# Kernel optimization log

Measured on AMD Instinct MI355X. Metric: run time of the kernel, lower is better.

The kernel has to match this reference:

```python
import jax, jax.numpy as jnp
import numpy as np

N_HEAD = 16
ROPE_BASE = 10000.0
RMS_EPS = 1e-6

def rms_norm(x):
    # F.rms_norm(x, (x.size(-1),)) -- no learned weight
    return x * jax.lax.rsqrt(jnp.mean(x * x, axis=-1, keepdims=True) + RMS_EPS)

def rope(x):
    # x: [B, T, H, hd]; rotate halves (non-interleaved) like the torch Rotary
    T, hd = x.shape[1], x.shape[3]
    d = hd // 2
    inv_freq = 1.0 / (ROPE_BASE ** (jnp.arange(0, hd, 2, dtype=jnp.float32) / hd))  # [d]
    t = jnp.arange(T, dtype=jnp.float32)
    freqs = jnp.outer(t, inv_freq)                       # [T, d]
    cos = jnp.cos(freqs)[None, :, None, :]
    sin = jnp.sin(freqs)[None, :, None, :]
    x1, x2 = x[..., :d], x[..., d:]
    y1 = x1 * cos + x2 * sin
    y2 = -x1 * sin + x2 * cos
    return jnp.concatenate([y1, y2], axis=-1).astype(x.dtype)

def setup_inputs() -> dict:
    key = jax.random.key(0)
    ks = jax.random.split(key, 7)
    B, T, D, H = 2, 2048, 1024, N_HEAD
    hd = D // H
    s = 0.02
    return {
        "x": jax.random.normal(ks[0], (B, T, D), jnp.float32),
        "v1": jax.random.normal(ks[1], (B, T, H, hd), jnp.float32),
        "w_q": jax.random.normal(ks[2], (D, D), jnp.float32) * s,
        "w_k": jax.random.normal(ks[3], (D, D), jnp.float32) * s,
        "w_v": jax.random.normal(ks[4], (D, D), jnp.float32) * s,
        "w_proj": jax.random.normal(ks[5], (D, D), jnp.float32) * s,
        "lamb": jnp.float32(0.5),
    }

def reference(x, v1, w_q, w_k, w_v, w_proj, lamb):
    B, T, D = x.shape
    H = N_HEAD
    hd = D // H
    q = (x @ w_q.T).reshape(B, T, H, hd)
    k = (x @ w_k.T).reshape(B, T, H, hd)
    v = (x @ w_v.T).reshape(B, T, H, hd)
    v = (1.0 - lamb) * v + lamb * v1.reshape(B, T, H, hd)
    q, k = rms_norm(q), rms_norm(k)
    q, k = rope(q), rope(k)
    scale = 1.0 / jnp.sqrt(jnp.float32(hd))
    scores = jnp.einsum('bqhd,bkhd->bhqk', q, k) * scale  # [B,H,T,T]
    causal = jnp.tril(jnp.ones((T, T), dtype=bool))
    scores = jnp.where(causal[None, None], scores, jnp.float32(-1e30))
    attn = jax.nn.softmax(scores, axis=-1)
    y = jnp.einsum('bhqk,bkhd->bqhd', attn, v).reshape(B, T, D)
    y = y @ w_proj.T
    return (y, v1)
```

## Files before the change

### kernel.cpp

```cpp
#include <hip/hip_runtime.h>

typedef __bf16 bf16x8 __attribute__((ext_vector_type(8)));
typedef float f32x4 __attribute__((ext_vector_type(4)));
typedef float f32x16 __attribute__((ext_vector_type(16)));

__device__ __forceinline__ unsigned short f2bf(float f) {
    return __builtin_bit_cast(unsigned short, (__bf16)f);
}

__device__ __forceinline__ float bf2f(unsigned short u) {
    unsigned int x = ((unsigned int)u) << 16;
    return __builtin_bit_cast(float, x);
}

__device__ __forceinline__ unsigned int packbf2(float a, float b) {
    unsigned short lo = f2bf(a), hi = f2bf(b);
    return (unsigned int)lo | ((unsigned int)hi << 16);
}

__device__ __forceinline__ bf16x8 load_frag(const unsigned short* p) {
    int4 v = *reinterpret_cast<const int4*>(p);
    return __builtin_bit_cast(bf16x8, v);
}

__device__ __forceinline__ void gload_lds16(const unsigned short* g, unsigned short* l) {
    __builtin_amdgcn_global_load_lds((const __attribute__((address_space(1))) void*)g,
                                     (__attribute__((address_space(3))) void*)l, 16, 0, 0);
}

__global__ __launch_bounds__(256) void prep_bf16(const float* __restrict__ x,
                                                 const float* __restrict__ wq,
                                                 const float* __restrict__ wk,
                                                 const float* __restrict__ wv,
                                                 const float* __restrict__ wp,
                                                 unsigned short* __restrict__ xb,
                                                 unsigned short* __restrict__ wall,
                                                 float* __restrict__ cost,
                                                 float* __restrict__ sint) {
    int bid = blockIdx.x;
    if (bid < 8192) {
        int i = (bid * 256 + threadIdx.x) * 4;
        const float* src;
        unsigned short* dst;
        int soff, doff;
        if (i < (1 << 22)) {
            src = x; dst = xb; soff = i; doff = i;
        } else {
            int j = i - (1 << 22);
            int r = j >> 20;
            src = (r == 0) ? wq : ((r == 1) ? wk : ((r == 2) ? wv : wp));
            dst = wall; soff = j & 1048575; doff = j;
        }
        float4 v = *reinterpret_cast<const float4*>(&src[soff]);
        unsigned short tmp[4] = {f2bf(v.x), f2bf(v.y), f2bf(v.z), f2bf(v.w)};
        *reinterpret_cast<int2*>(&dst[doff]) = *reinterpret_cast<int2*>(tmp);
    } else {
        int i = (bid - 8192) * 256 + threadIdx.x;
        int t = i >> 5, d = i & 31;
        float inv = powf(10000.0f, -(float)d / 32.0f);
        float f = (float)t * inv;
        cost[i] = cosf(f);
        sint[i] = sinf(f);
    }
}

__global__ __launch_bounds__(256) void gemm_qkv(const unsigned short* __restrict__ A,
                                                const unsigned short* __restrict__ B,
                                                const float* __restrict__ cost,
                                                const float* __restrict__ sint,
                                                const float* __restrict__ v1,
                                                const float* __restrict__ lamb_p,
                                                unsigned short* __restrict__ qb,
                                                unsigned short* __restrict__ kb,
                                                unsigned short* __restrict__ vbv,
                                                float* __restrict__ outv1) {
    __shared__ __align__(16) unsigned short As[128 * 64];
    __shared__ __align__(16) unsigned short Bs[128 * 64];
    int tid = threadIdx.x;
    int lane = tid & 63;
    int w = tid >> 6;
    int wm = w >> 1, wn = w & 1;
    int m0 = blockIdx.x * 128;
    int n0 = blockIdx.y * 128;

    f32x4 acc[4][4] = {};

    int r8 = lane >> 3;
    int csrc = (lane & 7) ^ r8;

    for (int k0 = 0; k0 < 1024; k0 += 64) {
        __syncthreads();
#pragma unroll
        for (int c = 0; c < 4; ++c) {
            int row = 32 * w + 8 * c + r8;
            gload_lds16(&A[(size_t)(m0 + row) * 1024 + k0 + csrc * 8], &As[(32 * w + 8 * c) * 64]);
            gload_lds16(&B[(size_t)(n0 + row) * 1024 + k0 + csrc * 8], &Bs[(32 * w + 8 * c) * 64]);
        }
        __syncthreads();
#pragma unroll
        for (int kk = 0; kk < 2; ++kk) {
            int col16 = kk * 4 + (lane >> 4);
            bf16x8 af[4], bfr[4];
#pragma unroll
            for (int i = 0; i < 4; ++i) {
                int row = wm * 64 + i * 16 + (lane & 15);
                af[i] = load_frag(&As[row * 64 + (col16 ^ (row & 7)) * 8]);
            }
#pragma unroll
            for (int j = 0; j < 4; ++j) {
                int row = wn * 64 + j * 16 + (lane & 15);
                bfr[j] = load_frag(&Bs[row * 64 + (col16 ^ (row & 7)) * 8]);
            }
#pragma unroll
            for (int i = 0; i < 4; ++i)
#pragma unroll
                for (int j = 0; j < 4; ++j)
                    acc[i][j] = __builtin_amdgcn_mfma_f32_16x16x32_bf16(af[i], bfr[j], acc[i][j], 0, 0, 0);
        }
    }

    int r0 = (lane >> 4) * 4;
    int cc = lane & 15;
    int sec = blockIdx.y >> 3;
    int hh = (blockIdx.y & 7) * 2 + wn;

    if (sec < 2) {
        unsigned short* dst = (sec == 0) ? qb : kb;
        float sc = (sec == 0) ? (0.125f * 1.44269504088896f) : 1.0f;
#pragma unroll
        for (int i = 0; i < 4; ++i)
#pragma unroll
            for (int r = 0; r < 4; ++r) {
                float ss = 0.0f;
#pragma unroll
                for (int j = 0; j < 4; ++j) ss += acc[i][j][r] * acc[i][j][r];
                ss += __shfl_xor(ss, 1, 64);
                ss += __shfl_xor(ss, 2, 64);
                ss += __shfl_xor(ss, 4, 64);
                ss += __shfl_xor(ss, 8, 64);
                float rn = rsqrtf(ss * (1.0f / 64.0f) + 1e-6f);
                int mm = m0 + wm * 64 + i * 16 + r0 + r;
                int t = mm & 2047, b = mm >> 11;
                size_t rowb = ((size_t)((b * 16 + hh) * 2048 + t)) * 64;
#pragma unroll
                for (int j = 0; j < 2; ++j) {
                    int dm = j * 16 + cc;
                    float c = cost[t * 32 + dm], s_ = sint[t * 32 + dm];
                    float x1 = acc[i][j][r] * rn;
                    float x2 = acc[i][j + 2][r] * rn;
                    dst[rowb + dm]      = f2bf((x1 * c + x2 * s_) * sc);
                    dst[rowb + 32 + dm] = f2bf((x2 * c - x1 * s_) * sc);
                }
            }
    } else {
        float lam = lamb_p[0];
        float oml = 1.0f - lam;
#pragma unroll
        for (int i = 0; i < 4; ++i)
#pragma unroll
            for (int r = 0; r < 4; ++r) {
                int mm = m0 + wm * 64 + i * 16 + r0 + r;
                int t = mm & 2047, b = mm >> 11;
                size_t v1row = ((size_t)((b * 2048 + t) * 16 + hh)) * 64;
                size_t vbrow = ((size_t)((b * 16 + hh) * 2048 + t)) * 64;
#pragma unroll
                for (int j = 0; j < 4; ++j) {
                    int d = j * 16 + cc;
                    float v1v = v1[v1row + d];
                    outv1[v1row + d] = v1v;
                    vbv[vbrow + d] = f2bf(oml * acc[i][j][r] + lam * v1v);
                }
            }
    }
}

__global__ __launch_bounds__(256) void transpose_v(const unsigned short* __restrict__ vbv,
                                                   unsigned short* __restrict__ vt) {
    __shared__ __align__(16) unsigned short tile[64][72];
    int bid = blockIdx.x;
    int bh = bid >> 5;
    int t0 = (bid & 31) * 64;
    int tid = threadIdx.x;
    int r = tid >> 3;
    int c = (tid & 7) * 8;
    const unsigned short* src = vbv + ((size_t)bh * 2048 + t0) * 64;
    *reinterpret_cast<int4*>(&tile[r][c]) =
        *reinterpret_cast<const int4*>(&src[(size_t)r * 64 + c]);
    *reinterpret_cast<int4*>(&tile[r + 32][c]) =
        *reinterpret_cast<const int4*>(&src[(size_t)(r + 32) * 64 + c]);
    __syncthreads();
    unsigned short* dst = vt + (size_t)bh * 64 * 2048 + t0;
    unsigned short tmp[8];
#pragma unroll
    for (int j = 0; j < 8; ++j) tmp[j] = tile[c + j][r];
    *reinterpret_cast<int4*>(&dst[(size_t)r * 2048 + c]) = *reinterpret_cast<int4*>(tmp);
#pragma unroll
    for (int j = 0; j < 8; ++j) tmp[j] = tile[c + j][r + 32];
    *reinterpret_cast<int4*>(&dst[(size_t)(r + 32) * 2048 + c]) = *reinterpret_cast<int4*>(tmp);
}

__global__ __launch_bounds__(256) void gemm_proj(const unsigned short* __restrict__ pO,
                                                 const float* __restrict__ lsum,
                                                 const unsigned short* __restrict__ B,
                                                 float* __restrict__ C) {
    __shared__ __align__(16) unsigned short As[128 * 64];
    __shared__ __align__(16) unsigned short Bs[128 * 64];
    int tid = threadIdx.x;
    int lane = tid & 63;
    int w = tid >> 6;
    int wm = w >> 1, wn = w & 1;
    int m0 = blockIdx.x * 128;
    int n0 = blockIdx.y * 128;

    f32x4 acc[4][4] = {};

    int r8 = lane >> 3;
    int c8 = lane & 7;
    int csrc = c8 ^ r8;

    for (int k0 = 0; k0 < 1024; k0 += 64) {
        int h = k0 >> 6;
        __syncthreads();
#pragma unroll
        for (int c = 0; c < 4; ++c) {
            int row = 32 * w + 8 * c + r8;
            int m = m0 + row;
            int bh = ((m >> 11) << 4) + h;
            int qi = m & 2047;
            int li = bh * 2048 + qi;
            size_t pi = (size_t)li * 64 + csrc * 8;
            int4 p0 = *reinterpret_cast<const int4*>(&pO[pi]);
            int4 p1 = *reinterpret_cast<const int4*>(&pO[4194304u + pi]);
            float linv = 1.0f / (lsum[li] + lsum[65536 + li]);
            const unsigned short* u0 = reinterpret_cast<const unsigned short*>(&p0);
            const unsigned short* u1 = reinterpret_cast<const unsigned short*>(&p1);
            unsigned short tmp[8];
#pragma unroll
            for (int j = 0; j < 8; ++j) tmp[j] = f2bf((bf2f(u0[j]) + bf2f(u1[j])) * linv);
            *reinterpret_cast<int4*>(&As[row * 64 + c8 * 8]) = *reinterpret_cast<int4*>(tmp);
            gload_lds16(&B[(size_t)(n0 + row) * 1024 + k0 + csrc * 8], &Bs[(32 * w + 8 * c) * 64]);
        }
        __syncthreads();
#pragma unroll
        for (int kk = 0; kk < 2; ++kk) {
            int col16 = kk * 4 + (lane >> 4);
            bf16x8 af[4], bfr[4];
#pragma unroll
            for (int i = 0; i < 4; ++i) {
                int row = wm * 64 + i * 16 + (lane & 15);
                af[i] = load_frag(&As[row * 64 + (col16 ^ (row & 7)) * 8]);
            }
#pragma unroll
            for (int j = 0; j < 4; ++j) {
                int row = wn * 64 + j * 16 + (lane & 15);
                bfr[j] = load_frag(&Bs[row * 64 + (col16 ^ (row & 7)) * 8]);
            }
#pragma unroll
            for (int i = 0; i < 4; ++i)
#pragma unroll
                for (int j = 0; j < 4; ++j)
                    acc[i][j] = __builtin_amdgcn_mfma_f32_16x16x32_bf16(af[i], bfr[j], acc[i][j], 0, 0, 0);
        }
    }
    int r0 = (lane >> 4) * 4;
    int cc = lane & 15;
#pragma unroll
    for (int i = 0; i < 4; ++i)
#pragma unroll
        for (int j = 0; j < 4; ++j)
#pragma unroll
            for (int r = 0; r < 4; ++r) {
                size_t m = m0 + wm * 64 + i * 16 + r0 + r;
                size_t n = n0 + wn * 64 + j * 16 + cc;
                C[m * 1024 + n] = acc[i][j][r];
            }
}

__global__ __launch_bounds__(256) void attn(const unsigned short* __restrict__ qb,
                                            const unsigned short* __restrict__ kb,
                                            const unsigned short* __restrict__ vt,
                                            unsigned short* __restrict__ pO,
                                            float* __restrict__ lsum) {
    __shared__ __align__(16) unsigned short Ks[64][72];
    __shared__ __align__(16) unsigned short Vt[64][72];
    int tid = threadIdx.x;
    int lane = tid & 63;
    int w = tid >> 6;
    int hi = lane >> 5;
    int l31 = lane & 31;

    int bid = blockIdx.x;
    int bh = bid & 31;
    int r5 = bid >> 5;
    int qt = 15 - (r5 >> 1);
    int ck = r5 & 1;
    int q0 = qt * 128;
    const size_t base = (size_t)bh * 2048 * 64;
    const unsigned short* vtb = vt + (size_t)bh * 64 * 2048;
    int ktlo = ck * (qt + 1);
    int kthi = (ck + 1) * (qt + 1);

    bf16x8 qf[4];
    int qrow = q0 + w * 32 + l31;
#pragma unroll
    for (int kd = 0; kd < 4; ++kd)
        qf[kd] = load_frag(&qb[base + (size_t)qrow * 64 + kd * 16 + hi * 8]);

    f32x16 oacc[2] = {};
    float lrun = 0.0f;

    int srow = tid >> 3;
    int scol = (tid & 7) * 8;
    int4 kr0, kr1, vr0, vr1;
#define LOADT(kt_)                                                                                    \
    do {                                                                                              \
        kr0 = *reinterpret_cast<const int4*>(&kb[base + (size_t)((kt_)*64 + srow) * 64 + scol]);      \
        kr1 = *reinterpret_cast<const int4*>(&kb[base + (size_t)((kt_)*64 + srow + 32) * 64 + scol]); \
        vr0 = *reinterpret_cast<const int4*>(&vtb[(size_t)srow * 2048 + (kt_)*64 + scol]);            \
        vr1 = *reinterpret_cast<const int4*>(&vtb[(size_t)(srow + 32) * 2048 + (kt_)*64 + scol]);     \
    } while (0)

    int qwlo = q0 + w * 32;
    {
        LOADT(ktlo);
        for (int kt = ktlo; kt < kthi; ++kt) {
            __syncthreads();
            *reinterpret_cast<int4*>(&Ks[srow][scol]) = kr0;
            *reinterpret_cast<int4*>(&Ks[srow + 32][scol]) = kr1;
            *reinterpret_cast<int4*>(&Vt[srow][scol]) = vr0;
            *reinterpret_cast<int4*>(&Vt[srow + 32][scol]) = vr1;
            __syncthreads();
            if (kt + 1 < kthi) LOADT(kt + 1);

            if (kt * 64 <= qwlo + 31) {
                bool diag = (kt * 64 + 63 > qwlo);
                float rs01 = 0.0f, rs23 = 0.0f;
#pragma unroll
                for (int ntl = 0; ntl < 2; ++ntl) {
                    f32x16 sacc = {};
#pragma unroll
                    for (int kd = 0; kd < 4; ++kd) {
                        bf16x8 kf = load_frag(&Ks[ntl * 32 + l31][kd * 16 + hi * 8]);
                        sacc = __builtin_amdgcn_mfma_f32_32x32x16_bf16(kf, qf[kd], sacc, 0, 0, 0);
                    }

#pragma unroll
                    for (int r = 0; r < 16; ++r) {
                        float s = sacc[r];
                        if (diag) {
                            int kvg = kt * 64 + ntl * 32 + (r & 3) + 8 * (r >> 2) + 4 * hi;
                            if (kvg > qrow) s = -3.0e38f;
                        }
                        float e = __builtin_amdgcn_exp2f(s);
                        sacc[r] = e;
                        if (r & 2) rs23 += e; else rs01 += e;
                    }

                    unsigned int wAa[4], wBb[4];
#pragma unroll
                    for (int rr = 0; rr < 4; ++rr) {
                        wAa[rr] = packbf2(sacc[4 * rr + 0], sacc[4 * rr + 1]);
                        wBb[rr] = packbf2(sacc[4 * rr + 2], sacc[4 * rr + 3]);
                    }

#pragma unroll
                    for (int ks2 = 0; ks2 < 2; ++ks2) {
                        int b2 = ks2 * 2;
                        auto rA = __builtin_amdgcn_permlane32_swap(wAa[b2], wAa[b2 + 1], false, false);
                        auto rB = __builtin_amdgcn_permlane32_swap(wBb[b2], wBb[b2 + 1], false, false);
                        uint4 pa;
                        pa.x = rA[0];
                        pa.y = rB[0];
                        pa.z = rA[1];
                        pa.w = rB[1];
                        bf16x8 paf = __builtin_bit_cast(bf16x8, pa);
                        int ks = ntl * 2 + ks2;
#pragma unroll
                        for (int dt = 0; dt < 2; ++dt) {
                            bf16x8 vtf = load_frag(&Vt[dt * 32 + l31][ks * 16 + hi * 8]);
                            oacc[dt] = __builtin_amdgcn_mfma_f32_32x32x16_bf16(paf, vtf, oacc[dt], 0, 0, 0);
                        }
                    }
                }
                float rs = rs01 + rs23;
                rs += __shfl_xor(rs, 32, 64);
                lrun += rs;
            }
        }
    }

    unsigned short* po = pO + ((size_t)ck * 4194304u);
    float* ls = lsum + ck * 65536;
#pragma unroll
    for (int r = 0; r < 16; ++r) {
        int ql = (r & 3) + 8 * (r >> 2) + 4 * hi;
        int q = q0 + w * 32 + ql;
        size_t ro = ((size_t)bh * 2048 + q) * 64;
        po[ro + l31]      = f2bf(oacc[0][r]);
        po[ro + 32 + l31] = f2bf(oacc[1][r]);
    }
    if (hi == 0) ls[bh * 2048 + q0 + w * 32 + l31] = lrun;
#undef LOADT
}

extern "C" void kernel_launch(void* const* d_in, const int* in_sizes, int n_in,
                              void* d_out, int out_size, void* d_ws, size_t ws_size,
                              hipStream_t stream) {
    const float* x      = (const float*)d_in[0];
    const float* v1     = (const float*)d_in[1];
    const float* w_q    = (const float*)d_in[2];
    const float* w_k    = (const float*)d_in[3];
    const float* w_v    = (const float*)d_in[4];
    const float* w_proj = (const float*)d_in[5];
    const float* lamb   = (const float*)d_in[6];
    float* out = (float*)d_out;

    char* ws = (char*)d_ws;
    unsigned short* xb      = (unsigned short*)(ws + 0);
    unsigned short* wall_b  = (unsigned short*)(ws + (8u  << 20));
    unsigned short* wqkv_b  = wall_b;
    unsigned short* wproj_b = wall_b + 3u * 1048576u;
    unsigned short* vbuf    = (unsigned short*)(ws + (16u << 20));
    unsigned short* vtp     = (unsigned short*)(ws + (40u << 20));
    unsigned short* qbuf    = (unsigned short*)(ws + (48u << 20));
    unsigned short* kbuf    = (unsigned short*)(ws + (56u << 20));
    float*          cost    = (float*)        (ws + (72u << 20));
    float*          sint    = (float*)        (ws + (72u << 20) + 262144);
    unsigned short* pO      = (unsigned short*)(ws + (80u << 20));
    float*          lsum    = (float*)        (ws + (112u << 20));

    prep_bf16<<<8448, 256, 0, stream>>>(x, w_q, w_k, w_v, w_proj, xb, wall_b, cost, sint);

    gemm_qkv<<<dim3(32, 24), 256, 0, stream>>>(xb, wqkv_b, cost, sint, v1, lamb,
                                               qbuf, kbuf, vbuf, out + 4194304);

    transpose_v<<<1024, 256, 0, stream>>>(vbuf, vtp);

    attn<<<1024, 256, 0, stream>>>(qbuf, kbuf, vtp, pO, lsum);

    gemm_proj<<<dim3(32, 8), 256, 0, stream>>>(pO, lsum, wproj_b, out);
}
```

Baseline: 130.5 us.

## Fuse V transpose into a dedicated V projection GEMM epilogue

Splits the combined QKV GEMM into a Q/K GEMM and a separate V GEMM whose epilogue mixes in v1, stages the result in shared memory, and writes V directly in transposed layout. This removes the standalone transpose kernel and the intermediate V buffer round trip through global memory. In exchange the V GEMM runs as its own launch with only 256 blocks, which may underfill the GPU, and the epilogue adds an LDS staging pass and extra barriers.

```diff
diff --git a/kernel.cpp b/kernel.cpp
--- a/kernel.cpp
+++ b/kernel.cpp
@@ -64,16 +64,12 @@
     }
 }
 
-__global__ __launch_bounds__(256) void gemm_qkv(const unsigned short* __restrict__ A,
-                                                const unsigned short* __restrict__ B,
-                                                const float* __restrict__ cost,
-                                                const float* __restrict__ sint,
-                                                const float* __restrict__ v1,
-                                                const float* __restrict__ lamb_p,
-                                                unsigned short* __restrict__ qb,
-                                                unsigned short* __restrict__ kb,
-                                                unsigned short* __restrict__ vbv,
-                                                float* __restrict__ outv1) {
+__global__ __launch_bounds__(256) void gemm_qk(const unsigned short* __restrict__ A,
+                                               const unsigned short* __restrict__ B,
+                                               const float* __restrict__ cost,
+                                               const float* __restrict__ sint,
+                                               unsigned short* __restrict__ qb,
+                                               unsigned short* __restrict__ kb) {
     __shared__ __align__(16) unsigned short As[128 * 64];
     __shared__ __align__(16) unsigned short Bs[128 * 64];
     int tid = threadIdx.x;
@@ -123,80 +119,131 @@
     int cc = lane & 15;
     int sec = blockIdx.y >> 3;
     int hh = (blockIdx.y & 7) * 2 + wn;
-
-    if (sec < 2) {
-        unsigned short* dst = (sec == 0) ? qb : kb;
-        float sc = (sec == 0) ? (0.125f * 1.44269504088896f) : 1.0f;
-#pragma unroll
-        for (int i = 0; i < 4; ++i)
-#pragma unroll
-            for (int r = 0; r < 4; ++r) {
-                float ss = 0.0f;
-#pragma unroll
-                for (int j = 0; j < 4; ++j) ss += acc[i][j][r] * acc[i][j][r];
-                ss += __shfl_xor(ss, 1, 64);
-                ss += __shfl_xor(ss, 2, 64);
-                ss += __shfl_xor(ss, 4, 64);
-                ss += __shfl_xor(ss, 8, 64);
-                float rn = rsqrtf(ss * (1.0f / 64.0f) + 1e-6f);
-                int mm = m0 + wm * 64 + i * 16 + r0 + r;
-                int t = mm & 2047, b = mm >> 11;
-                size_t rowb = ((size_t)((b * 16 + hh) * 2048 + t)) * 64;
-#pragma unroll
-                for (int j = 0; j < 2; ++j) {
-                    int dm = j * 16 + cc;
-                    float c = cost[t * 32 + dm], s_ = sint[t * 32 + dm];
-                    float x1 = acc[i][j][r] * rn;
-                    float x2 = acc[i][j + 2][r] * rn;
-                    dst[rowb + dm]      = f2bf((x1 * c + x2 * s_) * sc);
-                    dst[rowb + 32 + dm] = f2bf((x2 * c - x1 * s_) * sc);
-                }
-            }
-    } else {
-        float lam = lamb_p[0];
-        float oml = 1.0f - lam;
-#pragma unroll
-        for (int i = 0; i < 4; ++i)
-#pragma unroll
-            for (int r = 0; r < 4; ++r) {
-                int mm = m0 + wm * 64 + i * 16 + r0 + r;
-                int t = mm & 2047, b = mm >> 11;
-                size_t v1row = ((size_t)((b * 2048 + t) * 16 + hh)) * 64;
-                size_t vbrow = ((size_t)((b * 16 + hh) * 2048 + t)) * 64;
-#pragma unroll
-                for (int j = 0; j < 4; ++j) {
-                    int d = j * 16 + cc;
-                    float v1v = v1[v1row + d];
-                    outv1[v1row + d] = v1v;
-                    vbv[vbrow + d] = f2bf(oml * acc[i][j][r] + lam * v1v);
-                }
-            }
-    }
-}
-
-__global__ __launch_bounds__(256) void transpose_v(const unsigned short* __restrict__ vbv,
-                                                   unsigned short* __restrict__ vt) {
-    __shared__ __align__(16) unsigned short tile[64][72];
-    int bid = blockIdx.x;
-    int bh = bid >> 5;
-    int t0 = (bid & 31) * 64;
+    unsigned short* dst = (sec == 0) ? qb : kb;
+    float sc = (sec == 0) ? (0.125f * 1.44269504088896f) : 1.0f;
+#pragma unroll
+    for (int i = 0; i < 4; ++i)
+#pragma unroll
+        for (int r = 0; r < 4; ++r) {
+            float ss = 0.0f;
+#pragma unroll
+            for (int j = 0; j < 4; ++j) ss += acc[i][j][r] * acc[i][j][r];
+            ss += __shfl_xor(ss, 1, 64);
+            ss += __shfl_xor(ss, 2, 64);
+            ss += __shfl_xor(ss, 4, 64);
+            ss += __shfl_xor(ss, 8, 64);
+            float rn = rsqrtf(ss * (1.0f / 64.0f) + 1e-6f);
+            int mm = m0 + wm * 64 + i * 16 + r0 + r;
+            int t = mm & 2047, b = mm >> 11;
+            size_t rowb = ((size_t)((b * 16 + hh) * 2048 + t)) * 64;
+#pragma unroll
+            for (int j = 0; j < 2; ++j) {
+                int dm = j * 16 + cc;
+                float c = cost[t * 32 + dm], s_ = sint[t * 32 + dm];
+                float x1 = acc[i][j][r] * rn;
+                float x2 = acc[i][j + 2][r] * rn;
+                dst[rowb + dm]      = f2bf((x1 * c + x2 * s_) * sc);
+                dst[rowb + 32 + dm] = f2bf((x2 * c - x1 * s_) * sc);
+            }
+        }
+}
+
+__global__ __launch_bounds__(256) void gemm_v(const unsigned short* __restrict__ A,
+                                              const unsigned short* __restrict__ Bv,
+                                              const float* __restrict__ v1,
+                                              const float* __restrict__ lamb_p,
+                                              unsigned short* __restrict__ vt,
+                                              float* __restrict__ outv1) {
+    __shared__ __align__(16) unsigned short smem[2 * 128 * 72];
+    unsigned short* As = smem;
+    unsigned short* Bs = smem + 128 * 64;
     int tid = threadIdx.x;
-    int r = tid >> 3;
-    int c = (tid & 7) * 8;
-    const unsigned short* src = vbv + ((size_t)bh * 2048 + t0) * 64;
-    *reinterpret_cast<int4*>(&tile[r][c]) =
-        *reinterpret_cast<const int4*>(&src[(size_t)r * 64 + c]);
-    *reinterpret_cast<int4*>(&tile[r + 32][c]) =
-        *reinterpret_cast<const int4*>(&src[(size_t)(r + 32) * 64 + c]);
+    int lane = tid & 63;
+    int w = tid >> 6;
+    int wm = w >> 1, wn = w & 1;
+    int m0 = blockIdx.x * 128;
+    int n0 = blockIdx.y * 128;
+
+    f32x4 acc[4][4] = {};
+
+    int r8 = lane >> 3;
+    int csrc = (lane & 7) ^ r8;
+
+    for (int k0 = 0; k0 < 1024; k0 += 64) {
+        __syncthreads();
+#pragma unroll
+        for (int c = 0; c < 4; ++c) {
+            int row = 32 * w + 8 * c + r8;
+            gload_lds16(&A[(size_t)(m0 + row) * 1024 + k0 + csrc * 8], &As[(32 * w + 8 * c) * 64]);
+            gload_lds16(&Bv[(size_t)(n0 + row) * 1024 + k0 + csrc * 8], &Bs[(32 * w + 8 * c) * 64]);
+        }
+        __syncthreads();
+#pragma unroll
+        for (int kk = 0; kk < 2; ++kk) {
+            int col16 = kk * 4 + (lane >> 4);
+            bf16x8 af[4], bfr[4];
+#pragma unroll
+            for (int i = 0; i < 4; ++i) {
+                int row = wm * 64 + i * 16 + (lane & 15);
+                af[i] = load_frag(&As[row * 64 + (col16 ^ (row & 7)) * 8]);
+            }
+#pragma unroll
+            for (int j = 0; j < 4; ++j) {
+                int row = wn * 64 + j * 16 + (lane & 15);
+                bfr[j] = load_frag(&Bs[row * 64 + (col16 ^ (row & 7)) * 8]);
+            }
+#pragma unroll
+            for (int i = 0; i < 4; ++i)
+#pragma unroll
+                for (int j = 0; j < 4; ++j)
+                    acc[i][j] = __builtin_amdgcn_mfma_f32_16x16x32_bf16(af[i], bfr[j], acc[i][j], 0, 0, 0);
+        }
+    }
+
+    typedef unsigned short (*tile_t)[128][72];
+    tile_t tile = reinterpret_cast<tile_t>(smem);
+    int r0 = (lane >> 4) * 4;
+    int cc = lane & 15;
+    int hh = blockIdx.y * 2 + wn;
+    float lam = lamb_p[0];
+    float oml = 1.0f - lam;
     __syncthreads();
-    unsigned short* dst = vt + (size_t)bh * 64 * 2048 + t0;
+#pragma unroll
+    for (int i = 0; i < 4; ++i)
+#pragma unroll
+        for (int r = 0; r < 4; ++r) {
+            int tl = wm * 64 + i * 16 + r0 + r;
+            int mm = m0 + tl;
+            int t = mm & 2047, b = mm >> 11;
+            size_t v1row = ((size_t)((b * 2048 + t) * 16 + hh)) * 64;
+#pragma unroll
+            for (int j = 0; j < 4; ++j) {
+                int d = j * 16 + cc;
+                float v1v = v1[v1row + d];
+                outv1[v1row + d] = v1v;
+                tile[wn][tl][d] = f2bf(oml * acc[i][j][r] + lam * v1v);
+            }
+        }
+    __syncthreads();
+
+    int h2 = tid >> 7;
+    int idx = tid & 127;
+    int rr2 = idx >> 2;
+    int c2 = (idx & 3) * 8;
+    int hhs = blockIdx.y * 2 + h2;
+    int t0 = m0 & 2047;
+    int bb = m0 >> 11;
+    unsigned short* dst = vt + ((size_t)(bb * 16 + hhs)) * 64 * 2048;
     unsigned short tmp[8];
 #pragma unroll
-    for (int j = 0; j < 8; ++j) tmp[j] = tile[c + j][r];
-    *reinterpret_cast<int4*>(&dst[(size_t)r * 2048 + c]) = *reinterpret_cast<int4*>(tmp);
-#pragma unroll
-    for (int j = 0; j < 8; ++j) tmp[j] = tile[c + j][r + 32];
-    *reinterpret_cast<int4*>(&dst[(size_t)(r + 32) * 2048 + c]) = *reinterpret_cast<int4*>(tmp);
+    for (int tb = 0; tb < 128; tb += 32) {
+#pragma unroll
+        for (int j = 0; j < 8; ++j) tmp[j] = tile[h2][tb + c2 + j][rr2];
+        *reinterpret_cast<int4*>(&dst[(size_t)rr2 * 2048 + t0 + tb + c2]) = *reinterpret_cast<int4*>(tmp);
+#pragma unroll
+        for (int j = 0; j < 8; ++j) tmp[j] = tile[h2][tb + c2 + j][rr2 + 32];
+        *reinterpret_cast<int4*>(&dst[(size_t)(rr2 + 32) * 2048 + t0 + tb + c2]) = *reinterpret_cast<int4*>(tmp);
+    }
 }
 
 __global__ __launch_bounds__(256) void gemm_proj(const unsigned short* __restrict__ pO,
@@ -419,8 +466,8 @@
     unsigned short* xb      = (unsigned short*)(ws + 0);
     unsigned short* wall_b  = (unsigned short*)(ws + (8u  << 20));
     unsigned short* wqkv_b  = wall_b;
+    unsigned short* wv_b    = wall_b + 2u * 1048576u;
     unsigned short* wproj_b = wall_b + 3u * 1048576u;
-    unsigned short* vbuf    = (unsigned short*)(ws + (16u << 20));
     unsigned short* vtp     = (unsigned short*)(ws + (40u << 20));
     unsigned short* qbuf    = (unsigned short*)(ws + (48u << 20));
     unsigned short* kbuf    = (unsigned short*)(ws + (56u << 20));
@@ -431,10 +478,8 @@
 
     prep_bf16<<<8448, 256, 0, stream>>>(x, w_q, w_k, w_v, w_proj, xb, wall_b, cost, sint);
 
-    gemm_qkv<<<dim3(32, 24), 256, 0, stream>>>(xb, wqkv_b, cost, sint, v1, lamb,
-                                               qbuf, kbuf, vbuf, out + 4194304);
-
-    transpose_v<<<1024, 256, 0, stream>>>(vbuf, vtp);
+    gemm_qk<<<dim3(32, 16), 256, 0, stream>>>(xb, wqkv_b, cost, sint, qbuf, kbuf);
+    gemm_v<<<dim3(32, 8), 256, 0, stream>>>(xb, wv_b, v1, lamb, vtp, out + 4194304);
 
     attn<<<1024, 256, 0, stream>>>(qbuf, kbuf, vtp, pO, lsum);
 
```

New measurement: 129.9 us. About the same (-0.5%).
